# Performance work log

Hardware: AMD Instinct MI355X
Metric: run time of the kernel (lower is better)

Reference implementation:

```python
import jax, jax.numpy as jnp
import numpy as np

ALP = 2.2
BEL = 0.025


def _mlp2(x, W1, b1, W2, b2):
    # MLP([d_in, d_hid, d_out]): Linear -> ReLU -> Linear
    h = jax.nn.relu(x @ W1 + b1)
    return h @ W2 + b2


def _gate(p):
    # vectorized piecewise clamp: 0 below bel, 1 above 1/alp+bel, linear ramp between
    return jnp.where(p <= BEL, 0.0, jnp.where(p >= 1.0 / ALP + BEL, 1.0, ALP * (p - BEL)))


def setup_inputs() -> dict:
    key = jax.random.key(0)
    ks = jax.random.split(key, 8)
    insnum, E, d = 300, 89700, 512
    s = lambda fan: 1.0 / np.sqrt(fan)
    return {
        "obj_codes": jax.random.normal(ks[0], (insnum, d), dtype=jnp.float32),
        "pred_codes": jax.random.normal(ks[1], (E, d), dtype=jnp.float32),
        # pred_mlp_edge: MLP([512, 512, 512])
        "We1": jax.random.normal(ks[2], (d, d), dtype=jnp.float32) * s(d),
        "be1": jnp.zeros((d,), dtype=jnp.float32),
        "We2": jax.random.normal(ks[3], (d, d), dtype=jnp.float32) * s(d),
        "be2": jnp.zeros((d,), dtype=jnp.float32),
        # type_classifer: MLP([512, 128, 4])
        "Wt1": jax.random.normal(ks[4], (d, 128), dtype=jnp.float32) * s(d),
        "bt1": jnp.zeros((128,), dtype=jnp.float32),
        "Wt2": jax.random.normal(ks[5], (128, 4), dtype=jnp.float32) * s(128),
        "bt2": jnp.zeros((4,), dtype=jnp.float32),
    }


def reference(obj_codes, pred_codes, We1, be1, We2, be2, Wt1, bt1, Wt2, bt2):
    edge_embed = _mlp2(pred_codes, We1, be1, We2, be2)          # [E, 512]
    type_pred = _mlp2(edge_embed, Wt1, bt1, Wt2, bt2)           # [E, 4]
    type_output = jax.nn.softmax(type_pred, axis=1)             # [E, 4]
    none_w = type_output[:, 0]
    types_w = jnp.stack([1.0 - none_w, type_output[:, 1], type_output[:, 2], type_output[:, 3]], axis=0)  # [4, E]
    multiW = _gate(types_w)                                     # [4, E] (gated link/support/p/c weights)
    return types_w, multiW, type_output, edge_embed
```

## Files before the change

kernel.cpp:

```cpp
#include <hip/hip_runtime.h>
#include <math.h>


#define ALP 2.2f
#define BEL 0.025f
#define GATE_HI 0.4795454545454546f

typedef __attribute__((ext_vector_type(8))) short bf16x8;
typedef __attribute__((ext_vector_type(4))) float f32x4;

__device__ __forceinline__ unsigned short f2bf(float f) {
    unsigned int u = __float_as_uint(f);
    u = (u + 0x7FFF + ((u >> 16) & 1)) >> 16;
    return (unsigned short)u;
}

__device__ __forceinline__ void async_copy16(const unsigned short* g, unsigned short* l) {
    __builtin_amdgcn_global_load_lds(
        (const __attribute__((address_space(1))) unsigned int*)(g),
        (__attribute__((address_space(3))) unsigned int*)(l),
        16, 0, 0);
}

__global__ __launch_bounds__(256) void transpose_cvt(
    const float* __restrict__ W, unsigned short* __restrict__ Wt, int K, int N)
{
    __shared__ float t[32][33];
    const int bk = blockIdx.x * 32, bn = blockIdx.y * 32;
    const int tx = threadIdx.x & 31, ty = threadIdx.x >> 5;
#pragma unroll
    for (int i = 0; i < 32; i += 8)
        t[ty + i][tx] = W[(size_t)(bk + ty + i) * N + bn + tx];
    __syncthreads();
#pragma unroll
    for (int i = 0; i < 32; i += 8)
        Wt[(size_t)(bn + ty + i) * K + bk + tx] = f2bf(t[tx][ty + i]);
}

#define SMEM_BS    65536
#define SMEM_TOTAL 131072

__device__ __forceinline__ float gate_fn(float p) {
    if (p <= BEL) return 0.0f;
    if (p >= GATE_HI) return 1.0f;
    return ALP * (p - BEL);
}

__global__ __launch_bounds__(512, 2) void fused_mlp(
    const float* __restrict__ pred,
    const unsigned short* __restrict__ We1t, const float* __restrict__ be1,
    const unsigned short* __restrict__ We2t, const float* __restrict__ be2,
    const unsigned short* __restrict__ Wt1t, const float* __restrict__ bt1,
    const float* __restrict__ Wt2,  const float* __restrict__ bt2,
    float* __restrict__ out, int M)
{
    __shared__ __align__(16) unsigned char smem[SMEM_TOTAL];
    unsigned short* bigb = (unsigned short*)(smem);
    unsigned short* Bs   = (unsigned short*)(smem + SMEM_BS);
    float* T1s = (float*)(smem + SMEM_BS);
    float* Ws  = (float*)(smem + SMEM_BS + 33024);
    float* sm  = (float*)(smem + SMEM_BS + 33024 + 2048);

    const int tid  = threadIdx.x;
    const int lane = tid & 63;
    const int wave = tid >> 6;
    const int fm   = lane & 15;
    const int quad = lane >> 4;
    const int m0   = blockIdx.x * 64;

    float* EE = out + (size_t)12 * M;

    const int ecol  = fm;
    const int erow4 = quad * 4;
    const int wn    = wave * 64;

    f32x4 acc[4][4];
#pragma unroll
    for (int i = 0; i < 4; ++i)
#pragma unroll
        for (int j = 0; j < 4; ++j) acc[i][j] = (f32x4){0.f, 0.f, 0.f, 0.f};

#pragma unroll
    for (int i = 0; i < 4; ++i) {
        int c = i * 512 + tid;
        int r = c >> 2, q = c & 3;
        int qs = q ^ ((r >> 1) & 3);
        async_copy16(We1t + (size_t)r * 512 + qs * 8, Bs + c * 8);
    }
    {
        const int xr = tid >> 3;
        int grow = m0 + xr; if (grow >= M) grow = M - 1;
        const float* src = pred + (size_t)grow * 512;
        unsigned char* drow = (unsigned char*)bigb + xr * 1024;
        const int swz = (xr & 7) << 4;
#pragma unroll
        for (int j = 0; j < 8; ++j) {
            const int u = (tid & 7) + 8 * j;
            float4 a = *(const float4*)(src + u * 8);
            float4 b = *(const float4*)(src + u * 8 + 4);
            bf16x8 v;
            v[0] = (short)f2bf(a.x); v[1] = (short)f2bf(a.y);
            v[2] = (short)f2bf(a.z); v[3] = (short)f2bf(a.w);
            v[4] = (short)f2bf(b.x); v[5] = (short)f2bf(b.y);
            v[6] = (short)f2bf(b.z); v[7] = (short)f2bf(b.w);
            *(bf16x8*)(drow + ((u * 16) ^ swz)) = v;
        }
    }
    __syncthreads();

    for (int ks = 0; ks < 16; ++ks) {
        const int cur = ks & 1, nxt = cur ^ 1;
        if (ks < 15) {
#pragma unroll
            for (int i = 0; i < 4; ++i) {
                int c = i * 512 + tid;
                int r = c >> 2, q = c & 3;
                int qs = q ^ ((r >> 1) & 3);
                async_copy16(We1t + (size_t)r * 512 + (ks + 1) * 32 + qs * 8,
                             Bs + nxt * 16384 + c * 8);
            }
        }
        bf16x8 af[4], bfr[4];
        const unsigned char* bb = (const unsigned char*)Bs + cur * 32768;
#pragma unroll
        for (int i = 0; i < 4; ++i) {
            int r = i * 16 + fm;
            af[i] = *(const bf16x8*)((const unsigned char*)bigb + r * 1024 +
                                     ((ks * 64 + quad * 16) ^ ((r & 7) << 4)));
        }
#pragma unroll
        for (int j = 0; j < 4; ++j) {
            int r = wn + j * 16 + fm;
            bfr[j] = *(const bf16x8*)(bb + r * 64 + ((quad * 16) ^ (((r >> 1) & 3) << 4)));
        }
#pragma unroll
        for (int i = 0; i < 4; ++i)
#pragma unroll
            for (int j = 0; j < 4; ++j)
                acc[i][j] = __builtin_amdgcn_mfma_f32_16x16x32_bf16(
                    af[i], bfr[j], acc[i][j], 0, 0, 0);
        __syncthreads();
    }

    {
#pragma unroll
        for (int i = 0; i < 4; ++i) {
            int c = i * 512 + tid;
            int r = c >> 2, q = c & 3;
            int qs = q ^ ((r >> 1) & 3);
            async_copy16(We2t + (size_t)r * 512 + qs * 8, Bs + c * 8);
        }
#pragma unroll
        for (int j = 0; j < 4; ++j) {
            const int col = wn + j * 16 + ecol;
            const float bv = be1[col];
#pragma unroll
            for (int i = 0; i < 4; ++i)
#pragma unroll
                for (int rr = 0; rr < 4; ++rr) {
                    int row = i * 16 + erow4 + rr;
                    float v = fmaxf(acc[i][j][rr] + bv, 0.f);
                    *(unsigned short*)((unsigned char*)bigb + row * 1024 +
                                       ((col * 2) ^ ((row & 7) << 4))) = f2bf(v);
                }
        }
    }
    __syncthreads();

#pragma unroll
    for (int i = 0; i < 4; ++i)
#pragma unroll
        for (int j = 0; j < 4; ++j) acc[i][j] = (f32x4){0.f, 0.f, 0.f, 0.f};

    for (int ks = 0; ks < 16; ++ks) {
        const int cur = ks & 1, nxt = cur ^ 1;
        if (ks < 15) {
#pragma unroll
            for (int i = 0; i < 4; ++i) {
                int c = i * 512 + tid;
                int r = c >> 2, q = c & 3;
                int qs = q ^ ((r >> 1) & 3);
                async_copy16(We2t + (size_t)r * 512 + (ks + 1) * 32 + qs * 8,
                             Bs + nxt * 16384 + c * 8);
            }
        }
        bf16x8 af[4], bfr[4];
        const unsigned char* bb = (const unsigned char*)Bs + cur * 32768;
#pragma unroll
        for (int i = 0; i < 4; ++i) {
            int r = i * 16 + fm;
            af[i] = *(const bf16x8*)((const unsigned char*)bigb + r * 1024 +
                                     ((ks * 64 + quad * 16) ^ ((r & 7) << 4)));
        }
#pragma unroll
        for (int j = 0; j < 4; ++j) {
            int r = wn + j * 16 + fm;
            bfr[j] = *(const bf16x8*)(bb + r * 64 + ((quad * 16) ^ (((r >> 1) & 3) << 4)));
        }
#pragma unroll
        for (int i = 0; i < 4; ++i)
#pragma unroll
            for (int j = 0; j < 4; ++j)
                acc[i][j] = __builtin_amdgcn_mfma_f32_16x16x32_bf16(
                    af[i], bfr[j], acc[i][j], 0, 0, 0);
        __syncthreads();
    }

    {
        {
            int c = tid;
            int r = c >> 2, q = c & 3;
            int qs = q ^ ((r >> 1) & 3);
            async_copy16(Wt1t + (size_t)r * 512 + qs * 8, Bs + c * 8);
        }
#pragma unroll
        for (int j = 0; j < 4; ++j) {
            const int col = wn + j * 16 + ecol;
            const float bv = be2[col];
#pragma unroll
            for (int i = 0; i < 4; ++i)
#pragma unroll
                for (int rr = 0; rr < 4; ++rr) {
                    int row = i * 16 + erow4 + rr;
                    float v = acc[i][j][rr] + bv;
                    if (m0 + row < M)
                        EE[(size_t)(m0 + row) * 512 + col] = v;
                    *(unsigned short*)((unsigned char*)bigb + row * 1024 +
                                       ((col * 2) ^ ((row & 7) << 4))) = f2bf(v);
                }
        }
    }
    __syncthreads();

    f32x4 acc3[4];
#pragma unroll
    for (int i = 0; i < 4; ++i) acc3[i] = (f32x4){0.f, 0.f, 0.f, 0.f};
    const int wn3 = wave * 16;

    for (int ks = 0; ks < 16; ++ks) {
        const int cur = ks & 1, nxt = cur ^ 1;
        if (ks < 15) {
            int c = tid;
            int r = c >> 2, q = c & 3;
            int qs = q ^ ((r >> 1) & 3);
            async_copy16(Wt1t + (size_t)r * 512 + (ks + 1) * 32 + qs * 8,
                         Bs + nxt * 4096 + c * 8);
        }
        bf16x8 af[4], bfr3;
        const unsigned char* bb = (const unsigned char*)Bs + cur * 8192;
#pragma unroll
        for (int i = 0; i < 4; ++i) {
            int r = i * 16 + fm;
            af[i] = *(const bf16x8*)((const unsigned char*)bigb + r * 1024 +
                                     ((ks * 64 + quad * 16) ^ ((r & 7) << 4)));
        }
        {
            int r = wn3 + fm;
            bfr3 = *(const bf16x8*)(bb + r * 64 + ((quad * 16) ^ (((r >> 1) & 3) << 4)));
        }
#pragma unroll
        for (int i = 0; i < 4; ++i)
            acc3[i] = __builtin_amdgcn_mfma_f32_16x16x32_bf16(af[i], bfr3, acc3[i], 0, 0, 0);
        __syncthreads();
    }

    if (tid < 128) {
        float4 w = *(const float4*)&Wt2[tid * 4];
        *(float4*)&Ws[tid * 4] = w;
    }
    {
        const int col = wn3 + ecol;
        const float bv = bt1[col];
#pragma unroll
        for (int i = 0; i < 4; ++i)
#pragma unroll
            for (int rr = 0; rr < 4; ++rr) {
                int row = i * 16 + erow4 + rr;
                T1s[row * 129 + col] = fmaxf(acc3[i][rr] + bv, 0.f);
            }
    }
    __syncthreads();

    if (tid < 256) {
        const int row = tid & 63, col = tid >> 6;
        float d = bt2[col];
#pragma unroll
        for (int k = 0; k < 128; ++k)
            d = fmaf(T1s[row * 129 + k], Ws[k * 4 + col], d);
        sm[col * 64 + row] = d;
    }
    __syncthreads();

    if (tid < 64) {
        int r = m0 + tid;
        if (r < M) {
            float v0 = sm[0 * 64 + tid], v1 = sm[1 * 64 + tid];
            float v2 = sm[2 * 64 + tid], v3 = sm[3 * 64 + tid];
            float mx = fmaxf(fmaxf(v0, v1), fmaxf(v2, v3));
            float e0 = expf(v0 - mx), e1 = expf(v1 - mx);
            float e2 = expf(v2 - mx), e3 = expf(v3 - mx);
            float inv = 1.0f / (e0 + e1 + e2 + e3);
            float p0 = e0 * inv, p1 = e1 * inv, p2 = e2 * inv, p3 = e3 * inv;
            float tw0 = 1.0f - p0;

            float* TW = out;
            float* MW = out + (size_t)4 * M;
            float* TO = out + (size_t)8 * M;
            TW[0 * (size_t)M + r] = tw0;
            TW[1 * (size_t)M + r] = p1;
            TW[2 * (size_t)M + r] = p2;
            TW[3 * (size_t)M + r] = p3;
            MW[0 * (size_t)M + r] = gate_fn(tw0);
            MW[1 * (size_t)M + r] = gate_fn(p1);
            MW[2 * (size_t)M + r] = gate_fn(p2);
            MW[3 * (size_t)M + r] = gate_fn(p3);
            *(float4*)&TO[(size_t)r * 4] = make_float4(p0, p1, p2, p3);
        }
    }
}

extern "C" void kernel_launch(void* const* d_in, const int* in_sizes, int n_in,
                              void* d_out, int out_size, void* d_ws, size_t ws_size,
                              hipStream_t stream)
{
    const float* pred = (const float*)d_in[1];
    const float* We1  = (const float*)d_in[2];
    const float* be1  = (const float*)d_in[3];
    const float* We2  = (const float*)d_in[4];
    const float* be2  = (const float*)d_in[5];
    const float* Wt1  = (const float*)d_in[6];
    const float* bt1  = (const float*)d_in[7];
    const float* Wt2  = (const float*)d_in[8];
    const float* bt2  = (const float*)d_in[9];

    const int M = in_sizes[1] / 512;
    float* out = (float*)d_out;

    unsigned short* We1t = (unsigned short*)d_ws;
    unsigned short* We2t = We1t + 512 * 512;
    unsigned short* Wt1t = We2t + 512 * 512;

    dim3 blk(256);
    transpose_cvt<<<dim3(16, 16), blk, 0, stream>>>(We1, We1t, 512, 512);
    transpose_cvt<<<dim3(16, 16), blk, 0, stream>>>(We2, We2t, 512, 512);
    transpose_cvt<<<dim3(16, 4),  blk, 0, stream>>>(Wt1, Wt1t, 512, 128);

    const int mt = (M + 63) / 64;
    fused_mlp<<<dim3(mt), dim3(512), 0, stream>>>(
        pred, We1t, be1, We2t, be2, Wt1t, bt1, Wt2, bt2, out, M);
}
```

Measured before the change: 537.9 us.

## Triple-buffer weight staging with distance-2 prefetch, raw waitcnt barriers, retiled third GEMM

Moves weight staging from a double-buffered, distance-1 prefetch to a three-buffer, distance-2 async prefetch. Each k-step now ends with an explicit s_waitcnt vmcnt plus s_barrier instead of __syncthreads, and s_setprio is raised around the MFMA block. This is meant to hide global-to-LDS latency. The third GEMM (512->128) is retiled so each wave computes a 2x2 grid of fragments over 64-wide K stages, instead of one column strip over 16 narrow steps. The swizzle is simplified to a single-bit quad flip, the three weight transpose kernels are merged into one launch, and LDS grows to 160KB. The simpler swizzle risks more LDS bank conflicts on the strided A-operand reads.

```diff
diff --git a/kernel.cpp b/kernel.cpp
--- a/kernel.cpp
+++ b/kernel.cpp
@@ -22,11 +22,20 @@
         16, 0, 0);
 }
 
-__global__ __launch_bounds__(256) void transpose_cvt(
-    const float* __restrict__ W, unsigned short* __restrict__ Wt, int K, int N)
-{
+__global__ __launch_bounds__(256) void transpose_cvt_all(
+    const float* __restrict__ W0, const float* __restrict__ W1,
+    const float* __restrict__ W2,
+    unsigned short* __restrict__ T0, unsigned short* __restrict__ T1,
+    unsigned short* __restrict__ T2)
+{
+    const int z = blockIdx.z;
+    const float* W = (z == 0) ? W0 : (z == 1) ? W1 : W2;
+    unsigned short* T = (z == 0) ? T0 : (z == 1) ? T1 : T2;
+    const int N = (z == 2) ? 128 : 512;
+    const int bn = blockIdx.y * 32;
+    if (bn >= N) return;
     __shared__ float t[32][33];
-    const int bk = blockIdx.x * 32, bn = blockIdx.y * 32;
+    const int bk = blockIdx.x * 32;
     const int tx = threadIdx.x & 31, ty = threadIdx.x >> 5;
 #pragma unroll
     for (int i = 0; i < 32; i += 8)
@@ -34,16 +43,42 @@
     __syncthreads();
 #pragma unroll
     for (int i = 0; i < 32; i += 8)
-        Wt[(size_t)(bn + ty + i) * K + bk + tx] = f2bf(t[tx][ty + i]);
+        T[(size_t)(bn + ty + i) * 512 + bk + tx] = f2bf(t[tx][ty + i]);
 }
 
 #define SMEM_BS    65536
-#define SMEM_TOTAL 131072
+#define SMEM_TOTAL 163840
 
 __device__ __forceinline__ float gate_fn(float p) {
     if (p <= BEL) return 0.0f;
     if (p >= GATE_HI) return 1.0f;
     return ALP * (p - BEL);
+}
+
+__device__ __forceinline__ void stage_w32(const unsigned short* Wt, int k0,
+                                          unsigned char* smem, int bufbase, int tid)
+{
+#pragma unroll
+    for (int i = 0; i < 4; ++i) {
+        int c = i * 512 + tid;
+        int r = c >> 2, q = c & 3;
+        int qs = q ^ (((r >> 3) & 1) << 1);
+        async_copy16(Wt + (size_t)r * 512 + k0 + qs * 8,
+                     (unsigned short*)(smem + bufbase) + (size_t)c * 8);
+    }
+}
+
+__device__ __forceinline__ void stage_c64(const unsigned short* Wt, int k0,
+                                          unsigned char* smem, int bufbase, int tid)
+{
+#pragma unroll
+    for (int i = 0; i < 2; ++i) {
+        int c = i * 512 + tid;
+        int r = c >> 3, q = c & 7;
+        int qs = q ^ (((r >> 3) & 1) << 1);
+        async_copy16(Wt + (size_t)r * 512 + k0 + qs * 8,
+                     (unsigned short*)(smem + bufbase) + (size_t)c * 8);
+    }
 }
 
 __global__ __launch_bounds__(512, 2) void fused_mlp(
@@ -55,11 +90,9 @@
     float* __restrict__ out, int M)
 {
     __shared__ __align__(16) unsigned char smem[SMEM_TOTAL];
-    unsigned short* bigb = (unsigned short*)(smem);
-    unsigned short* Bs   = (unsigned short*)(smem + SMEM_BS);
     float* T1s = (float*)(smem + SMEM_BS);
     float* Ws  = (float*)(smem + SMEM_BS + 33024);
-    float* sm  = (float*)(smem + SMEM_BS + 33024 + 2048);
+    float* sm  = (float*)(smem + SMEM_BS + 35072);
 
     const int tid  = threadIdx.x;
     const int lane = tid & 63;
@@ -70,6 +103,8 @@
 
     float* EE = out + (size_t)12 * M;
 
+    const int sw   = ((fm >> 3) & 1) << 1;
+    const int qx16 = (quad ^ sw) << 4;
     const int ecol  = fm;
     const int erow4 = quad * 4;
     const int wn    = wave * 64;
@@ -80,19 +115,14 @@
 #pragma unroll
         for (int j = 0; j < 4; ++j) acc[i][j] = (f32x4){0.f, 0.f, 0.f, 0.f};
 
-#pragma unroll
-    for (int i = 0; i < 4; ++i) {
-        int c = i * 512 + tid;
-        int r = c >> 2, q = c & 3;
-        int qs = q ^ ((r >> 1) & 3);
-        async_copy16(We1t + (size_t)r * 512 + qs * 8, Bs + c * 8);
-    }
+    stage_w32(We1t, 0,  smem, SMEM_BS,         tid);
+    stage_w32(We1t, 32, smem, SMEM_BS + 32768, tid);
     {
         const int xr = tid >> 3;
         int grow = m0 + xr; if (grow >= M) grow = M - 1;
         const float* src = pred + (size_t)grow * 512;
-        unsigned char* drow = (unsigned char*)bigb + xr * 1024;
-        const int swz = (xr & 7) << 4;
+        unsigned char* drow = smem + xr * 1024;
+        const int xsw = ((xr >> 3) & 1) << 1;
 #pragma unroll
         for (int j = 0; j < 8; ++j) {
             const int u = (tid & 7) + 8 * j;
@@ -103,67 +133,55 @@
             v[2] = (short)f2bf(a.z); v[3] = (short)f2bf(a.w);
             v[4] = (short)f2bf(b.x); v[5] = (short)f2bf(b.y);
             v[6] = (short)f2bf(b.z); v[7] = (short)f2bf(b.w);
-            *(bf16x8*)(drow + ((u * 16) ^ swz)) = v;
-        }
-    }
-    __syncthreads();
-
+            *(bf16x8*)(drow + ((u ^ xsw) << 4)) = v;
+        }
+    }
+    __syncthreads();
+
+#pragma unroll
     for (int ks = 0; ks < 16; ++ks) {
-        const int cur = ks & 1, nxt = cur ^ 1;
-        if (ks < 15) {
-#pragma unroll
-            for (int i = 0; i < 4; ++i) {
-                int c = i * 512 + tid;
-                int r = c >> 2, q = c & 3;
-                int qs = q ^ ((r >> 1) & 3);
-                async_copy16(We1t + (size_t)r * 512 + (ks + 1) * 32 + qs * 8,
-                             Bs + nxt * 16384 + c * 8);
-            }
-        }
+        if (ks < 14)
+            stage_w32(We1t, (ks + 2) * 32, smem,
+                      SMEM_BS + ((ks + 2) % 3) * 32768, tid);
+        const unsigned char* bb = smem + SMEM_BS + (ks % 3) * 32768;
         bf16x8 af[4], bfr[4];
-        const unsigned char* bb = (const unsigned char*)Bs + cur * 32768;
 #pragma unroll
         for (int i = 0; i < 4; ++i) {
             int r = i * 16 + fm;
-            af[i] = *(const bf16x8*)((const unsigned char*)bigb + r * 1024 +
-                                     ((ks * 64 + quad * 16) ^ ((r & 7) << 4)));
+            af[i] = *(const bf16x8*)(smem + r * 1024 + ks * 64 + qx16);
         }
 #pragma unroll
         for (int j = 0; j < 4; ++j) {
             int r = wn + j * 16 + fm;
-            bfr[j] = *(const bf16x8*)(bb + r * 64 + ((quad * 16) ^ (((r >> 1) & 3) << 4)));
-        }
+            bfr[j] = *(const bf16x8*)(bb + r * 64 + qx16);
+        }
+        __builtin_amdgcn_s_setprio(1);
 #pragma unroll
         for (int i = 0; i < 4; ++i)
 #pragma unroll
             for (int j = 0; j < 4; ++j)
                 acc[i][j] = __builtin_amdgcn_mfma_f32_16x16x32_bf16(
                     af[i], bfr[j], acc[i][j], 0, 0, 0);
-        __syncthreads();
-    }
-
-    {
-#pragma unroll
-        for (int i = 0; i < 4; ++i) {
-            int c = i * 512 + tid;
-            int r = c >> 2, q = c & 3;
-            int qs = q ^ ((r >> 1) & 3);
-            async_copy16(We2t + (size_t)r * 512 + qs * 8, Bs + c * 8);
-        }
-#pragma unroll
-        for (int j = 0; j < 4; ++j) {
-            const int col = wn + j * 16 + ecol;
-            const float bv = be1[col];
-#pragma unroll
-            for (int i = 0; i < 4; ++i)
-#pragma unroll
-                for (int rr = 0; rr < 4; ++rr) {
-                    int row = i * 16 + erow4 + rr;
-                    float v = fmaxf(acc[i][j][rr] + bv, 0.f);
-                    *(unsigned short*)((unsigned char*)bigb + row * 1024 +
-                                       ((col * 2) ^ ((row & 7) << 4))) = f2bf(v);
-                }
-        }
+        __builtin_amdgcn_s_setprio(0);
+        if (ks < 14) { asm volatile("s_waitcnt vmcnt(4)\n\ts_barrier" ::: "memory"); }
+        else         { asm volatile("s_waitcnt vmcnt(0)\n\ts_barrier" ::: "memory"); }
+    }
+
+    stage_w32(We2t, 0,  smem, SMEM_BS,         tid);
+    stage_w32(We2t, 32, smem, SMEM_BS + 32768, tid);
+#pragma unroll
+    for (int j = 0; j < 4; ++j) {
+        const int col = wn + j * 16 + ecol;
+        const float bv = be1[col];
+#pragma unroll
+        for (int i = 0; i < 4; ++i)
+#pragma unroll
+            for (int rr = 0; rr < 4; ++rr) {
+                int row = i * 16 + erow4 + rr;
+                float v = fmaxf(acc[i][j][rr] + bv, 0.f);
+                *(unsigned short*)(smem + row * 1024 +
+                                   ((col * 2) ^ ((((row) >> 3) & 1) << 5))) = f2bf(v);
+            }
     }
     __syncthreads();
 
@@ -172,111 +190,109 @@
 #pragma unroll
         for (int j = 0; j < 4; ++j) acc[i][j] = (f32x4){0.f, 0.f, 0.f, 0.f};
 
+#pragma unroll
     for (int ks = 0; ks < 16; ++ks) {
-        const int cur = ks & 1, nxt = cur ^ 1;
-        if (ks < 15) {
-#pragma unroll
-            for (int i = 0; i < 4; ++i) {
-                int c = i * 512 + tid;
-                int r = c >> 2, q = c & 3;
-                int qs = q ^ ((r >> 1) & 3);
-                async_copy16(We2t + (size_t)r * 512 + (ks + 1) * 32 + qs * 8,
-                             Bs + nxt * 16384 + c * 8);
-            }
-        }
+        if (ks < 14)
+            stage_w32(We2t, (ks + 2) * 32, smem,
+                      SMEM_BS + ((ks + 2) % 3) * 32768, tid);
+        const unsigned char* bb = smem + SMEM_BS + (ks % 3) * 32768;
         bf16x8 af[4], bfr[4];
-        const unsigned char* bb = (const unsigned char*)Bs + cur * 32768;
 #pragma unroll
         for (int i = 0; i < 4; ++i) {
             int r = i * 16 + fm;
-            af[i] = *(const bf16x8*)((const unsigned char*)bigb + r * 1024 +
-                                     ((ks * 64 + quad * 16) ^ ((r & 7) << 4)));
+            af[i] = *(const bf16x8*)(smem + r * 1024 + ks * 64 + qx16);
         }
 #pragma unroll
         for (int j = 0; j < 4; ++j) {
             int r = wn + j * 16 + fm;
-            bfr[j] = *(const bf16x8*)(bb + r * 64 + ((quad * 16) ^ (((r >> 1) & 3) << 4)));
-        }
+            bfr[j] = *(const bf16x8*)(bb + r * 64 + qx16);
+        }
+        __builtin_amdgcn_s_setprio(1);
 #pragma unroll
         for (int i = 0; i < 4; ++i)
 #pragma unroll
             for (int j = 0; j < 4; ++j)
                 acc[i][j] = __builtin_amdgcn_mfma_f32_16x16x32_bf16(
                     af[i], bfr[j], acc[i][j], 0, 0, 0);
-        __syncthreads();
-    }
-
-    {
-        {
-            int c = tid;
-            int r = c >> 2, q = c & 3;
-            int qs = q ^ ((r >> 1) & 3);
-            async_copy16(Wt1t + (size_t)r * 512 + qs * 8, Bs + c * 8);
-        }
-#pragma unroll
-        for (int j = 0; j < 4; ++j) {
-            const int col = wn + j * 16 + ecol;
-            const float bv = be2[col];
-#pragma unroll
-            for (int i = 0; i < 4; ++i)
-#pragma unroll
-                for (int rr = 0; rr < 4; ++rr) {
-                    int row = i * 16 + erow4 + rr;
-                    float v = acc[i][j][rr] + bv;
-                    if (m0 + row < M)
-                        EE[(size_t)(m0 + row) * 512 + col] = v;
-                    *(unsigned short*)((unsigned char*)bigb + row * 1024 +
-                                       ((col * 2) ^ ((row & 7) << 4))) = f2bf(v);
-                }
-        }
-    }
-    __syncthreads();
-
-    f32x4 acc3[4];
-#pragma unroll
-    for (int i = 0; i < 4; ++i) acc3[i] = (f32x4){0.f, 0.f, 0.f, 0.f};
-    const int wn3 = wave * 16;
-
-    for (int ks = 0; ks < 16; ++ks) {
-        const int cur = ks & 1, nxt = cur ^ 1;
-        if (ks < 15) {
-            int c = tid;
-            int r = c >> 2, q = c & 3;
-            int qs = q ^ ((r >> 1) & 3);
-            async_copy16(Wt1t + (size_t)r * 512 + (ks + 1) * 32 + qs * 8,
-                         Bs + nxt * 4096 + c * 8);
-        }
-        bf16x8 af[4], bfr3;
-        const unsigned char* bb = (const unsigned char*)Bs + cur * 8192;
-#pragma unroll
-        for (int i = 0; i < 4; ++i) {
-            int r = i * 16 + fm;
-            af[i] = *(const bf16x8*)((const unsigned char*)bigb + r * 1024 +
-                                     ((ks * 64 + quad * 16) ^ ((r & 7) << 4)));
-        }
-        {
-            int r = wn3 + fm;
-            bfr3 = *(const bf16x8*)(bb + r * 64 + ((quad * 16) ^ (((r >> 1) & 3) << 4)));
-        }
+        __builtin_amdgcn_s_setprio(0);
+        if (ks < 14) { asm volatile("s_waitcnt vmcnt(4)\n\ts_barrier" ::: "memory"); }
+        else         { asm volatile("s_waitcnt vmcnt(0)\n\ts_barrier" ::: "memory"); }
+    }
+
+    stage_c64(Wt1t, 0,  smem, SMEM_BS,         tid);
+    stage_c64(Wt1t, 64, smem, SMEM_BS + 16384, tid);
+#pragma unroll
+    for (int j = 0; j < 4; ++j) {
+        const int col = wn + j * 16 + ecol;
+        const float bv = be2[col];
 #pragma unroll
         for (int i = 0; i < 4; ++i)
-            acc3[i] = __builtin_amdgcn_mfma_f32_16x16x32_bf16(af[i], bfr3, acc3[i], 0, 0, 0);
-        __syncthreads();
+#pragma unroll
+            for (int rr = 0; rr < 4; ++rr) {
+                int row = i * 16 + erow4 + rr;
+                float v = acc[i][j][rr] + bv;
+                if (m0 + row < M)
+                    EE[(size_t)(m0 + row) * 512 + col] = v;
+                *(unsigned short*)(smem + row * 1024 +
+                                   ((col * 2) ^ ((((row) >> 3) & 1) << 5))) = f2bf(v);
+            }
+    }
+    __syncthreads();
+
+    const int wr3 = wave >> 2;
+    const int wc3 = wave & 3;
+    f32x4 acc3[2][2];
+#pragma unroll
+    for (int i = 0; i < 2; ++i)
+#pragma unroll
+        for (int j = 0; j < 2; ++j) acc3[i][j] = (f32x4){0.f, 0.f, 0.f, 0.f};
+
+#pragma unroll
+    for (int ks = 0; ks < 8; ++ks) {
+        if (ks < 6)
+            stage_c64(Wt1t, (ks + 2) * 64, smem,
+                      SMEM_BS + ((ks + 2) % 3) * 16384, tid);
+        const unsigned char* bb = smem + SMEM_BS + (ks % 3) * 16384;
+#pragma unroll
+        for (int kk = 0; kk < 2; ++kk) {
+            bf16x8 a2[2], b2[2];
+#pragma unroll
+            for (int i = 0; i < 2; ++i) {
+                int r = wr3 * 32 + i * 16 + fm;
+                a2[i] = *(const bf16x8*)(smem + r * 1024 + (ks * 2 + kk) * 64 + qx16);
+            }
+#pragma unroll
+            for (int j = 0; j < 2; ++j) {
+                int r = wc3 * 32 + j * 16 + fm;
+                b2[j] = *(const bf16x8*)(bb + r * 128 + kk * 64 + qx16);
+            }
+            __builtin_amdgcn_s_setprio(1);
+#pragma unroll
+            for (int i = 0; i < 2; ++i)
+#pragma unroll
+                for (int j = 0; j < 2; ++j)
+                    acc3[i][j] = __builtin_amdgcn_mfma_f32_16x16x32_bf16(
+                        a2[i], b2[j], acc3[i][j], 0, 0, 0);
+            __builtin_amdgcn_s_setprio(0);
+        }
+        if (ks < 6) { asm volatile("s_waitcnt vmcnt(2)\n\ts_barrier" ::: "memory"); }
+        else        { asm volatile("s_waitcnt vmcnt(0)\n\ts_barrier" ::: "memory"); }
     }
 
     if (tid < 128) {
         float4 w = *(const float4*)&Wt2[tid * 4];
         *(float4*)&Ws[tid * 4] = w;
     }
-    {
-        const int col = wn3 + ecol;
+#pragma unroll
+    for (int j = 0; j < 2; ++j) {
+        const int col = wc3 * 32 + j * 16 + ecol;
         const float bv = bt1[col];
 #pragma unroll
-        for (int i = 0; i < 4; ++i)
+        for (int i = 0; i < 2; ++i)
 #pragma unroll
             for (int rr = 0; rr < 4; ++rr) {
-                int row = i * 16 + erow4 + rr;
-                T1s[row * 129 + col] = fmaxf(acc3[i][rr] + bv, 0.f);
+                int row = wr3 * 32 + i * 16 + erow4 + rr;
+                T1s[row * 129 + col] = fmaxf(acc3[i][j][rr] + bv, 0.f);
             }
     }
     __syncthreads();
@@ -340,10 +356,8 @@
     unsigned short* We2t = We1t + 512 * 512;
     unsigned short* Wt1t = We2t + 512 * 512;
 
-    dim3 blk(256);
-    transpose_cvt<<<dim3(16, 16), blk, 0, stream>>>(We1, We1t, 512, 512);
-    transpose_cvt<<<dim3(16, 16), blk, 0, stream>>>(We2, We2t, 512, 512);
-    transpose_cvt<<<dim3(16, 4),  blk, 0, stream>>>(Wt1, Wt1t, 512, 128);
+    transpose_cvt_all<<<dim3(16, 16, 3), dim3(256), 0, stream>>>(
+        We1, We2, Wt1, We1t, We2t, Wt1t);
 
     const int mt = (M + 63) / 64;
     fused_mlp<<<dim3(mt), dim3(512), 0, stream>>>(
```

Result: faster. 499.6 us (-7.1%).
